# Kernel tuning notes

Hardware: AMD Instinct MI355X
Metric: run time of the kernel (lower is better)

## Reference

```python
import jax, jax.numpy as jnp
import numpy as np

PAD = -2.0
EPS = 1e-6

def _ln(x, g, b):
    m = jnp.mean(x, axis=-1, keepdims=True)
    v = jnp.var(x, axis=-1, keepdims=True)
    return (x - m) * jax.lax.rsqrt(v + EPS) * g + b

def setup_inputs() -> dict:
    key = jax.random.key(0)
    ks = jax.random.split(key, 8)
    B, N, D, H, E = 4, 2048, 256, 4, 256
    x = jax.random.normal(ks[0], (B, N, D), dtype=jnp.float32)
    mask = jnp.where(jax.random.uniform(ks[1], (B, N)) < 0.9, 1.0, PAD).astype(jnp.float32)
    Wq = jax.random.normal(ks[2], (H, D, E), dtype=jnp.float32) * 0.02
    Wk = jax.random.normal(ks[3], (H, D, E), dtype=jnp.float32) * 0.02
    Wv = jax.random.normal(ks[4], (H, D, E), dtype=jnp.float32) * 0.02
    Wg = jax.random.uniform(ks[5], (H, D, E), dtype=jnp.float32, minval=-0.05, maxval=0.05)
    out_w = jax.random.normal(ks[6], (E * H, E), dtype=jnp.float32) * 0.02
    out_b = jnp.zeros((E,), dtype=jnp.float32)
    ones = jnp.ones((E,), dtype=jnp.float32)
    zeros = jnp.zeros((E,), dtype=jnp.float32)
    return {"x": x, "mask": mask, "Wq": Wq, "Wk": Wk, "Wv": Wv, "Wg": Wg,
            "out_w": out_w, "out_b": out_b,
            "g_in": ones, "b_in": zeros, "g_res": ones, "b_res": zeros,
            "g_out": ones, "b_out": zeros}

def reference(x, mask, Wq, Wk, Wv, Wg, out_w, out_b, g_in, b_in, g_res, b_res, g_out, b_out):
    B, N, D = x.shape
    H, _, E = Wq.shape
    m = jnp.where(mask == PAD, 0.0, 1.0)            # [B,N]
    x_norm = _ln(x, g_in, b_in)                      # [B,N,D]
    q = jnp.einsum('bnd,hde->hbne', x_norm, Wq)
    k = jnp.einsum('bmd,hde->hbme', x_norm, Wk)
    v = jnp.einsum('bmd,hde->hbme', x_norm, Wv)
    scale = 1.0 / jnp.sqrt(jnp.float32(E))
    att = jnp.einsum('hbne,hbme->hbnm', q, k) * scale  # [H,B,N,N]
    amask = m[:, :, None] * m[:, None, :]              # outer-product mask [B,N,N]
    att = att + (1.0 - amask)[None] * -1e9
    att = jax.nn.softmax(att, axis=-1) * amask[None]   # post-softmax renorm by mask
    out = jnp.einsum('hbnm,hbme->hbne', att, v)        # [H,B,N,E]
    gate = jax.nn.sigmoid(jnp.einsum('bnd,hde->hbne', x_norm, Wg))
    out = out * gate
    out = _ln(out + x[None], g_res, b_res)             # residual + LN per head
    out = jnp.transpose(out, (1, 2, 3, 0)).reshape(B, N, E * H)  # [B,N,E*H], e fastest then h
    out = out @ out_w + out_b + x
    out = _ln(out, g_out, b_out)
    out = out * m[:, :, None]
    return out
```

## Files before the change

### kernel.cpp

```cpp
#include <hip/hip_runtime.h>
#include <math.h>

#define B_SZ 4
#define N_SEQ 2048
#define D_DIM 256
#define H_HEADS 4
#define E_DIM 256
#define ROWS (B_SZ*N_SEQ)
#define PAD_TOK -2.0f
#define LN_EPS 1e-6f

typedef __attribute__((ext_vector_type(8))) short short8;
typedef __attribute__((ext_vector_type(4))) float f32x4;

static __device__ __forceinline__ unsigned short f2bf(float f){
  union { float f; unsigned u; } v; v.f = f;
  unsigned r = v.u + 0x7fffu + ((v.u >> 16) & 1u);
  return (unsigned short)(r >> 16);
}
static __device__ __forceinline__ float bf2f(unsigned short s){
  union { unsigned u; float f; } v; v.u = ((unsigned)s) << 16; return v.f;
}
static __device__ __forceinline__ f32x4 mfma16(short8 a, short8 b, f32x4 c){
  return __builtin_amdgcn_mfma_f32_16x16x32_bf16(a, b, c, 0, 0, 0);
}

#define GLOAD_LDS16(gsrc, ldst) \
  __builtin_amdgcn_global_load_lds((const __attribute__((address_space(1))) void*)(gsrc), \
                                   (__attribute__((address_space(3))) void*)(ldst), 16, 0, 0)

__global__ __launch_bounds__(256) void k_ln_in(
    const float* __restrict__ x, const float* __restrict__ mask,
    const float* __restrict__ g, const float* __restrict__ bta,
    unsigned short* __restrict__ xn, float* __restrict__ mval){
  int row = blockIdx.x * 4 + (threadIdx.x >> 6);
  int lane = threadIdx.x & 63;
  const float* xr = x + (size_t)row * D_DIM + lane * 4;
  f32x4 v = *reinterpret_cast<const f32x4*>(xr);
  float s = v[0]+v[1]+v[2]+v[3];
  float q = v[0]*v[0]+v[1]*v[1]+v[2]*v[2]+v[3]*v[3];
  #pragma unroll
  for (int m=1;m<64;m<<=1){ s += __shfl_xor(s,m,64); q += __shfl_xor(q,m,64); }
  float mean = s * (1.0f/D_DIM);
  float var  = q * (1.0f/D_DIM) - mean*mean;
  float rs = rsqrtf(var + LN_EPS);
  int c = lane*4;
  ushort4 o;
  o.x = f2bf((v[0]-mean)*rs*g[c+0] + bta[c+0]);
  o.y = f2bf((v[1]-mean)*rs*g[c+1] + bta[c+1]);
  o.z = f2bf((v[2]-mean)*rs*g[c+2] + bta[c+2]);
  o.w = f2bf((v[3]-mean)*rs*g[c+3] + bta[c+3]);
  *reinterpret_cast<ushort4*>(xn + (size_t)row*D_DIM + c) = o;
  if (lane == 0) mval[row] = (mask[row] == PAD_TOK) ? 0.0f : 1.0f;
}

__global__ __launch_bounds__(256) void k_prep_w(
    const float* __restrict__ Wq, const float* __restrict__ Wk,
    const float* __restrict__ Wv, const float* __restrict__ Wg,
    unsigned short* __restrict__ wt){
  int mat = blockIdx.z; int proj = mat >> 2, h = mat & 3;
  const float* W = (proj==0 ? Wq : (proj==1 ? Wk : (proj==2 ? Wv : Wg))) + (size_t)h * D_DIM * E_DIM;
  __shared__ float tile[64][65];
  int e0 = blockIdx.x*64, d0 = blockIdx.y*64;
  #pragma unroll
  for (int i=0;i<16;i++){
    int idx = threadIdx.x + i*256;
    int dl = idx >> 6, el = idx & 63;
    tile[dl][el] = W[(size_t)(d0+dl)*E_DIM + e0 + el];
  }
  __syncthreads();
  #pragma unroll
  for (int i=0;i<16;i++){
    int idx = threadIdx.x + i*256;
    int el = idx >> 6, dl = idx & 63;
    wt[((size_t)mat*E_DIM + e0+el)*D_DIM + d0+dl] = f2bf(tile[dl][el]);
  }
}

__global__ __launch_bounds__(256) void k_prep_ow(
    const float* __restrict__ out_w, unsigned short* __restrict__ owt){
  int c0 = blockIdx.x*64;
  int col0 = blockIdx.y*64;
  int hh = c0 >> 8; int e0 = c0 & 255;
  __shared__ float tile[64][65];
  #pragma unroll
  for (int i=0;i<16;i++){
    int idx = threadIdx.x + i*256;
    int el = idx>>6, cl = idx&63;
    tile[el][cl] = out_w[(size_t)((e0+el)*H_HEADS + hh)*E_DIM + col0+cl];
  }
  __syncthreads();
  #pragma unroll
  for (int i=0;i<16;i++){
    int idx = threadIdx.x + i*256;
    int cl = idx>>6, el = idx&63;
    owt[(size_t)(col0+cl)*1024 + c0 + el] = f2bf(tile[el][cl]);
  }
}

__global__ __launch_bounds__(256,2) void k_proj(
    const unsigned short* __restrict__ xn, const unsigned short* __restrict__ wt,
    unsigned short* __restrict__ qb, unsigned short* __restrict__ kb,
    unsigned short* __restrict__ vtb, unsigned short* __restrict__ gpb){
  int mat = blockIdx.y; int proj = mat >> 2, h = mat & 3;
  int wv = threadIdx.x >> 6, lane = threadIdx.x & 63;
  int lr = lane & 15, lg = lane >> 4;
  int r0 = blockIdx.x * 128 + wv * 32;
  const unsigned short* wm = wt + (size_t)mat * D_DIM * E_DIM;
  short8 a[2][8];
  #pragma unroll
  for (int qr=0;qr<2;qr++){
    const unsigned short* arow = xn + (size_t)(r0 + qr*16 + lr) * D_DIM + lg*8;
    #pragma unroll
    for (int kk=0;kk<8;kk++) a[qr][kk] = *reinterpret_cast<const short8*>(arow + kk*32);
  }
  unsigned short* outp = (proj==0 ? qb : (proj==1 ? kb : gpb)) + (size_t)h * ROWS * E_DIM;
  #pragma unroll 2
  for (int nt=0; nt<16; nt++){
    f32x4 acc0 = f32x4{0.f,0.f,0.f,0.f};
    f32x4 acc1 = f32x4{0.f,0.f,0.f,0.f};
    const unsigned short* brow = wm + (size_t)(nt*16 + lr) * D_DIM + lg*8;
    #pragma unroll
    for (int kk=0;kk<8;kk++){
      short8 bfrag = *reinterpret_cast<const short8*>(brow + kk*32);
      acc0 = mfma16(a[0][kk], bfrag, acc0);
      acc1 = mfma16(a[1][kk], bfrag, acc1);
    }
    int col = nt*16 + lr;
    if (proj == 2){
      #pragma unroll
      for (int r=0;r<4;r++){
        int row0 = r0 + lg*4 + r;
        int row1 = row0 + 16;
        vtb[(((size_t)(h*B_SZ + (row0>>11))*E_DIM + col) << 11) + (row0 & 2047)] = f2bf(acc0[r]);
        vtb[(((size_t)(h*B_SZ + (row1>>11))*E_DIM + col) << 11) + (row1 & 2047)] = f2bf(acc1[r]);
      }
    } else {
      #pragma unroll
      for (int r=0;r<4;r++){
        int row0 = r0 + lg*4 + r;
        outp[(size_t)row0*E_DIM + col] = f2bf(acc0[r]);
        outp[(size_t)(row0+16)*E_DIM + col] = f2bf(acc1[r]);
      }
    }
  }
}

__global__ __launch_bounds__(256,2) void k_attn(
    const unsigned short* __restrict__ qb, const unsigned short* __restrict__ kb,
    const unsigned short* __restrict__ vt, const unsigned short* __restrict__ gp,
    const float* __restrict__ mval, const float* __restrict__ x,
    const float* __restrict__ g_res, const float* __restrict__ b_res,
    unsigned short* __restrict__ attout){
  int hb = blockIdx.y; int h = hb >> 2, bb = hb & 3;
  int tid = threadIdx.x;
  int wv = tid >> 6, lane = tid & 63;
  int lr = lane & 15, lg = lane >> 4;
  int n0 = blockIdx.x * 64 + wv * 16;
  const unsigned short* qm = qb + ((size_t)h * ROWS + (size_t)bb * N_SEQ) * E_DIM;
  const unsigned short* km = kb + ((size_t)h * ROWS + (size_t)bb * N_SEQ) * E_DIM;
  const unsigned short* vm = vt + ((size_t)(h * B_SZ + bb)) * E_DIM * N_SEQ;
  const unsigned short* gpm = gp + ((size_t)h * ROWS + (size_t)bb * N_SEQ) * E_DIM;
  const float* mrow = mval + bb * N_SEQ;

  __shared__ alignas(16) unsigned short Klds[2][32*256];
  __shared__ alignas(16) unsigned short Vlds[2][256][36];
  __shared__ alignas(16) unsigned short Plds[4][16][40];

  short8 qf[8];
  {
    const unsigned short* qrow = qm + (size_t)(n0 + lr) * E_DIM + lg * 8;
    #pragma unroll
    for (int kk=0;kk<8;kk++) qf[kk] = *reinterpret_cast<const short8*>(qrow + kk*32);
  }
  f32x4 o[16];
  #pragma unroll
  for (int i=0;i<16;i++) o[i] = f32x4{0.f,0.f,0.f,0.f};
  float mrun[4], lrun[4];
  #pragma unroll
  for (int r=0;r<4;r++){ mrun[r] = -1.0e30f; lrun[r] = 0.f; }

  {
    const char* kg = (const char*)km;
    #pragma unroll
    for (int i=0;i<4;i++){
      int c = tid + i*256; int krow = c >> 5;
      unsigned off = ((unsigned)(c*16)) ^ ((unsigned)((krow&7)<<4));
      GLOAD_LDS16(kg + off, (char*)(&Klds[0][0]) + c*16);
    }
    const unsigned short* vr = vm + (size_t)tid * N_SEQ;
    short8 v0[4];
    #pragma unroll
    for (int i=0;i<4;i++) v0[i] = *reinterpret_cast<const short8*>(vr + i*8);
    #pragma unroll
    for (int i=0;i<4;i++) *reinterpret_cast<short8*>(&Vlds[0][tid][i*8]) = v0[i];
  }
  __syncthreads();

  int cur = 0;
  for (int kt=0; kt<N_SEQ/32; kt++){
    int nxt = cur ^ 1;
    short8 vreg[4];
    if (kt < N_SEQ/32 - 1){
      const char* kg = (const char*)(km + (size_t)(kt+1)*32*E_DIM);
      #pragma unroll
      for (int i=0;i<4;i++){
        int c = tid + i*256; int krow = c >> 5;
        unsigned off = ((unsigned)(c*16)) ^ ((unsigned)((krow&7)<<4));
        GLOAD_LDS16(kg + off, (char*)(&Klds[nxt][0]) + c*16);
      }
      const unsigned short* vr = vm + (size_t)tid * N_SEQ + (kt+1)*32;
      #pragma unroll
      for (int i=0;i<4;i++) vreg[i] = *reinterpret_cast<const short8*>(vr + i*8);
    }
    const char* kbase = (const char*)(&Klds[cur][0]);
    f32x4 s0 = f32x4{0.f,0.f,0.f,0.f}, s1v = f32x4{0.f,0.f,0.f,0.f};
    unsigned swz = (unsigned)((lr&7)<<4);
    #pragma unroll
    for (int kk=0;kk<8;kk++){
      short8 b0 = *reinterpret_cast<const short8*>(kbase + ((unsigned)(lr*512 + kk*64 + lg*16) ^ swz));
      short8 b1 = *reinterpret_cast<const short8*>(kbase + ((unsigned)((16+lr)*512 + kk*64 + lg*16) ^ swz));
      s0  = mfma16(qf[kk], b0, s0);
      s1v = mfma16(qf[kk], b1, s1v);
    }
    float mk0 = (mrow[kt*32 + lr] - 1.0f) * 1e9f;
    float mk1 = (mrow[kt*32 + 16 + lr] - 1.0f) * 1e9f;
    float p0[4], p1[4], tmax[4];
    #pragma unroll
    for (int r=0;r<4;r++){
      p0[r] = s0[r]*0.0625f + mk0;
      p1[r] = s1v[r]*0.0625f + mk1;
      tmax[r] = fmaxf(p0[r], p1[r]);
    }
    #pragma unroll
    for (int m=1;m<16;m<<=1){
      #pragma unroll
      for (int r=0;r<4;r++) tmax[r] = fmaxf(tmax[r], __shfl_xor(tmax[r], m, 16));
    }
    bool need = false;
    #pragma unroll
    for (int r=0;r<4;r++) need = need || (tmax[r] > mrun[r] + 8.0f);
    if (__any((int)need)){
      #pragma unroll
      for (int r=0;r<4;r++){
        float mnew = fmaxf(mrun[r], tmax[r]);
        float alpha = __expf(mrun[r] - mnew);
        mrun[r] = mnew;
        lrun[r] *= alpha;
        #pragma unroll
        for (int i=0;i<16;i++) o[i][r] *= alpha;
      }
    }
    float rsum[4];
    #pragma unroll
    for (int r=0;r<4;r++){
      p0[r] = __expf(p0[r] - mrun[r]);
      p1[r] = __expf(p1[r] - mrun[r]);
      rsum[r] = p0[r] + p1[r];
    }
    #pragma unroll
    for (int m=1;m<16;m<<=1){
      #pragma unroll
      for (int r=0;r<4;r++) rsum[r] += __shfl_xor(rsum[r], m, 16);
    }
    #pragma unroll
    for (int r=0;r<4;r++) lrun[r] += rsum[r];
    #pragma unroll
    for (int r=0;r<4;r++){
      Plds[wv][lg*4+r][lr]      = f2bf(p0[r]);
      Plds[wv][lg*4+r][16+lr]   = f2bf(p1[r]);
    }
    short8 pa = *reinterpret_cast<const short8*>(&Plds[wv][lr][lg*8]);
    #pragma unroll
    for (int et=0;et<16;et++){
      short8 bv = *reinterpret_cast<const short8*>(&Vlds[cur][et*16 + lr][lg*8]);
      o[et] = mfma16(pa, bv, o[et]);
    }
    if (kt < N_SEQ/32 - 1){
      #pragma unroll
      for (int i=0;i<4;i++) *reinterpret_cast<short8*>(&Vlds[nxt][tid][i*8]) = vreg[i];
    }
    __syncthreads();
    cur = nxt;
  }
  float inv[4], mm_[4], rs_[4];
  #pragma unroll
  for (int r=0;r<4;r++) inv[r] = (lrun[r] > 0.f) ? (1.0f / lrun[r]) : 0.f;
  float s1_[4] = {0,0,0,0}, s2_[4] = {0,0,0,0};
  #pragma unroll
  for (int et=0;et<16;et++){
    int col = et*16 + lr;
    #pragma unroll
    for (int r=0;r<4;r++){
      int n = n0 + lg*4 + r;
      float ov = o[et][r] * inv[r];
      float gpre = bf2f(gpm[(size_t)n*E_DIM + col]);
      float gate = 1.0f / (1.0f + __expf(-gpre));
      float val = ov * gate + x[((size_t)(bb*N_SEQ + n))*D_DIM + col];
      o[et][r] = val;
      s1_[r] += val; s2_[r] += val*val;
    }
  }
  #pragma unroll
  for (int m=1;m<16;m<<=1){
    #pragma unroll
    for (int r=0;r<4;r++){ s1_[r] += __shfl_xor(s1_[r], m, 16); s2_[r] += __shfl_xor(s2_[r], m, 16); }
  }
  #pragma unroll
  for (int r=0;r<4;r++){
    float mean = s1_[r] * (1.0f/E_DIM);
    float var  = s2_[r] * (1.0f/E_DIM) - mean*mean;
    mm_[r] = mean; rs_[r] = rsqrtf(var + LN_EPS);
  }
  #pragma unroll
  for (int et=0;et<16;et++){
    int col = et*16 + lr;
    float gr = g_res[col], br = b_res[col];
    #pragma unroll
    for (int r=0;r<4;r++){
      int n = n0 + lg*4 + r;
      float y = (o[et][r] - mm_[r]) * rs_[r] * gr + br;
      attout[((size_t)(bb*N_SEQ + n))*1024 + h*256 + col] = f2bf(y);
    }
  }
}

__global__ __launch_bounds__(128) void k_final(
    const unsigned short* __restrict__ attout, const unsigned short* __restrict__ owt,
    const float* __restrict__ out_b, const float* __restrict__ x,
    const float* __restrict__ g_out, const float* __restrict__ b_out,
    const float* __restrict__ mval, float* __restrict__ out){
  int wv = threadIdx.x >> 6, lane = threadIdx.x & 63;
  int lr = lane & 15, lg = lane >> 4;
  int r0 = blockIdx.x * 32 + wv*16;
  f32x4 acc[16];
  #pragma unroll
  for (int i=0;i<16;i++) acc[i] = f32x4{0.f,0.f,0.f,0.f};
  const unsigned short* arow = attout + (size_t)(r0 + lr)*1024 + lg*8;
  for (int kg=0; kg<4; kg++){
    short8 a[8];
    #pragma unroll
    for (int kk=0;kk<8;kk++) a[kk] = *reinterpret_cast<const short8*>(arow + kg*256 + kk*32);
    #pragma unroll
    for (int nt=0;nt<16;nt++){
      const unsigned short* brow = owt + (size_t)(nt*16 + lr)*1024 + kg*256 + lg*8;
      #pragma unroll
      for (int kk=0;kk<8;kk++){
        short8 bfrag = *reinterpret_cast<const short8*>(brow + kk*32);
        acc[nt] = mfma16(a[kk], bfrag, acc[nt]);
      }
    }
  }
  float s1_[4]={0,0,0,0}, s2_[4]={0,0,0,0};
  #pragma unroll
  for (int nt=0;nt<16;nt++){
    int col = nt*16 + lr;
    float ob = out_b[col];
    #pragma unroll
    for (int r=0;r<4;r++){
      int row = r0 + lg*4 + r;
      float val = acc[nt][r] + ob + x[(size_t)row*D_DIM + col];
      acc[nt][r] = val;
      s1_[r]+=val; s2_[r]+=val*val;
    }
  }
  #pragma unroll
  for (int m=1;m<16;m<<=1){
    #pragma unroll
    for (int r=0;r<4;r++){ s1_[r]+=__shfl_xor(s1_[r],m,16); s2_[r]+=__shfl_xor(s2_[r],m,16); }
  }
  float mm_[4], rs_[4];
  #pragma unroll
  for (int r=0;r<4;r++){
    float mean = s1_[r]*(1.0f/E_DIM);
    float var  = s2_[r]*(1.0f/E_DIM) - mean*mean;
    mm_[r]=mean; rs_[r]=rsqrtf(var + LN_EPS);
  }
  #pragma unroll
  for (int nt=0;nt<16;nt++){
    int col = nt*16 + lr;
    float gg = g_out[col], bb2 = b_out[col];
    #pragma unroll
    for (int r=0;r<4;r++){
      int row = r0 + lg*4 + r;
      float y = ((acc[nt][r]-mm_[r])*rs_[r]*gg + bb2) * mval[row];
      out[(size_t)row*E_DIM + col] = y;
    }
  }
}

extern "C" void kernel_launch(void* const* d_in, const int* in_sizes, int n_in,
                              void* d_out, int out_size, void* d_ws, size_t ws_size,
                              hipStream_t stream) {
  const float* x     = (const float*)d_in[0];
  const float* mask  = (const float*)d_in[1];
  const float* Wq    = (const float*)d_in[2];
  const float* Wk    = (const float*)d_in[3];
  const float* Wv    = (const float*)d_in[4];
  const float* Wg    = (const float*)d_in[5];
  const float* out_w = (const float*)d_in[6];
  const float* out_b = (const float*)d_in[7];
  const float* g_in  = (const float*)d_in[8];
  const float* b_in  = (const float*)d_in[9];
  const float* g_res = (const float*)d_in[10];
  const float* b_res = (const float*)d_in[11];
  const float* g_out = (const float*)d_in[12];
  const float* b_out = (const float*)d_in[13];

  char* ws = (char*)d_ws;
  size_t off = 0;
  unsigned short* xn   = (unsigned short*)(ws + off); off += (size_t)ROWS * D_DIM * 2;
  float*          mval = (float*)(ws + off);          off += (size_t)ROWS * 4;
  unsigned short* wt   = (unsigned short*)(ws + off); off += (size_t)16 * D_DIM * E_DIM * 2;
  unsigned short* owt  = (unsigned short*)(ws + off); off += (size_t)E_DIM * 1024 * 2;
  unsigned short* qb   = (unsigned short*)(ws + off); off += (size_t)H_HEADS * ROWS * E_DIM * 2;
  unsigned short* kb   = (unsigned short*)(ws + off); off += (size_t)H_HEADS * ROWS * E_DIM * 2;
  unsigned short* vtb  = (unsigned short*)(ws + off); off += (size_t)H_HEADS * ROWS * E_DIM * 2;
  unsigned short* gpb  = (unsigned short*)(ws + off); off += (size_t)H_HEADS * ROWS * E_DIM * 2;
  unsigned short* attout = (unsigned short*)(ws + off); off += (size_t)ROWS * 1024 * 2;

  k_ln_in<<<dim3(ROWS/4), dim3(256), 0, stream>>>(x, mask, g_in, b_in, xn, mval);
  k_prep_w<<<dim3(4,4,16), dim3(256), 0, stream>>>(Wq, Wk, Wv, Wg, wt);
  k_prep_ow<<<dim3(16,4), dim3(256), 0, stream>>>(out_w, owt);
  k_proj<<<dim3(ROWS/128, 16), dim3(256), 0, stream>>>(xn, wt, qb, kb, vtb, gpb);
  k_attn<<<dim3(N_SEQ/64, H_HEADS*B_SZ), dim3(256), 0, stream>>>(qb, kb, vtb, gpb, mval, x, g_res, b_res, attout);
  k_final<<<dim3(ROWS/32), dim3(128), 0, stream>>>(attout, owt, out_b, x, g_out, b_out, mval, (float*)d_out);
}
```

Measured before the change: 364.5 us.

## Process 32 query rows per wave in attention, load V via direct LDS DMA

Each wave now handles two 16-row query groups, so every K and V fragment read from LDS feeds two MFMAs. This halves K/V global and LDS traffic per query row, and the grid shrinks to 256 blocks. V tiles are now staged with swizzled global-to-LDS loads instead of register round-trips, and blocks are remapped so neighbouring block ids share the same head and batch for L2 reuse. In exchange, register pressure doubles (launch bounds drop to 1 block per CU), and 256 blocks on a large GPU may leave CUs underused.

New measurement: 401.3 us. +10.1%, slower.

```diff
diff --git a/kernel.cpp b/kernel.cpp
--- a/kernel.cpp
+++ b/kernel.cpp
@@ -146,183 +146,234 @@
   }
 }
 
-__global__ __launch_bounds__(256,2) void k_attn(
+__global__ __launch_bounds__(256,1) void k_attn(
     const unsigned short* __restrict__ qb, const unsigned short* __restrict__ kb,
     const unsigned short* __restrict__ vt, const unsigned short* __restrict__ gp,
     const float* __restrict__ mval, const float* __restrict__ x,
     const float* __restrict__ g_res, const float* __restrict__ b_res,
     unsigned short* __restrict__ attout){
-  int hb = blockIdx.y; int h = hb >> 2, bb = hb & 3;
+  int id = blockIdx.x;
+  int hb = (id & 7) + ((id >> 7) << 3);
+  int h = hb >> 2, bbx = hb & 3;
+  int nblk = (id >> 3) & 15;
   int tid = threadIdx.x;
   int wv = tid >> 6, lane = tid & 63;
   int lr = lane & 15, lg = lane >> 4;
-  int n0 = blockIdx.x * 64 + wv * 16;
-  const unsigned short* qm = qb + ((size_t)h * ROWS + (size_t)bb * N_SEQ) * E_DIM;
-  const unsigned short* km = kb + ((size_t)h * ROWS + (size_t)bb * N_SEQ) * E_DIM;
-  const unsigned short* vm = vt + ((size_t)(h * B_SZ + bb)) * E_DIM * N_SEQ;
-  const unsigned short* gpm = gp + ((size_t)h * ROWS + (size_t)bb * N_SEQ) * E_DIM;
-  const float* mrow = mval + bb * N_SEQ;
+  int n0 = nblk * 128 + wv * 32;
+  const unsigned short* qm = qb + ((size_t)h * ROWS + (size_t)bbx * N_SEQ) * E_DIM;
+  const unsigned short* km = kb + ((size_t)h * ROWS + (size_t)bbx * N_SEQ) * E_DIM;
+  const unsigned short* vm = vt + ((size_t)(h * B_SZ + bbx)) * E_DIM * N_SEQ;
+  const unsigned short* gpm = gp + ((size_t)h * ROWS + (size_t)bbx * N_SEQ) * E_DIM;
+  const float* mrow = mval + bbx * N_SEQ;
 
   __shared__ alignas(16) unsigned short Klds[2][32*256];
-  __shared__ alignas(16) unsigned short Vlds[2][256][36];
-  __shared__ alignas(16) unsigned short Plds[4][16][40];
-
-  short8 qf[8];
+  __shared__ alignas(16) unsigned short Vlds[2][256*32];
+  __shared__ alignas(16) unsigned short Plds[4][32][40];
+
+  short8 qf0[8], qf1[8];
   {
-    const unsigned short* qrow = qm + (size_t)(n0 + lr) * E_DIM + lg * 8;
-    #pragma unroll
-    for (int kk=0;kk<8;kk++) qf[kk] = *reinterpret_cast<const short8*>(qrow + kk*32);
-  }
-  f32x4 o[16];
-  #pragma unroll
-  for (int i=0;i<16;i++) o[i] = f32x4{0.f,0.f,0.f,0.f};
-  float mrun[4], lrun[4];
-  #pragma unroll
-  for (int r=0;r<4;r++){ mrun[r] = -1.0e30f; lrun[r] = 0.f; }
-
-  {
-    const char* kg = (const char*)km;
-    #pragma unroll
-    for (int i=0;i<4;i++){
-      int c = tid + i*256; int krow = c >> 5;
-      unsigned off = ((unsigned)(c*16)) ^ ((unsigned)((krow&7)<<4));
-      GLOAD_LDS16(kg + off, (char*)(&Klds[0][0]) + c*16);
-    }
-    const unsigned short* vr = vm + (size_t)tid * N_SEQ;
-    short8 v0[4];
-    #pragma unroll
-    for (int i=0;i<4;i++) v0[i] = *reinterpret_cast<const short8*>(vr + i*8);
-    #pragma unroll
-    for (int i=0;i<4;i++) *reinterpret_cast<short8*>(&Vlds[0][tid][i*8]) = v0[i];
-  }
+    const unsigned short* qr0 = qm + (size_t)(n0 + lr) * E_DIM + lg * 8;
+    const unsigned short* qr1 = qm + (size_t)(n0 + 16 + lr) * E_DIM + lg * 8;
+    #pragma unroll
+    for (int kk=0;kk<8;kk++){
+      qf0[kk] = *reinterpret_cast<const short8*>(qr0 + kk*32);
+      qf1[kk] = *reinterpret_cast<const short8*>(qr1 + kk*32);
+    }
+  }
+  f32x4 o0[16], o1[16];
+  #pragma unroll
+  for (int i=0;i<16;i++){ o0[i] = f32x4{0.f,0.f,0.f,0.f}; o1[i] = f32x4{0.f,0.f,0.f,0.f}; }
+  float mr0[4], lr0_[4], mr1[4], lr1_[4];
+  #pragma unroll
+  for (int r=0;r<4;r++){ mr0[r] = -1.0e30f; lr0_[r] = 0.f; mr1[r] = -1.0e30f; lr1_[r] = 0.f; }
+
+  #define STAGE_K(buf, kt_) { \
+    const char* kgb = (const char*)(km + (size_t)(kt_)*32*E_DIM); \
+    _Pragma("unroll") \
+    for (int i=0;i<4;i++){ \
+      int c = tid + i*256; int krow = c >> 5; \
+      unsigned off = ((unsigned)(c*16)) ^ ((unsigned)((krow&7)<<4)); \
+      GLOAD_LDS16(kgb + off, (char*)(&Klds[buf][0]) + c*16); \
+    } }
+  #define STAGE_V(buf, kt_) { \
+    const char* vgb = (const char*)vm; \
+    _Pragma("unroll") \
+    for (int i=0;i<4;i++){ \
+      int c = tid + i*256; int e = c >> 2; \
+      unsigned w = (unsigned)(((c&3)*16) ^ ((e&3)<<4)); \
+      GLOAD_LDS16(vgb + (size_t)e*(N_SEQ*2) + (size_t)(kt_)*64 + w, \
+                  (char*)(&Vlds[buf][0]) + c*16); \
+    } }
+
+  STAGE_K(0, 0)
+  STAGE_V(0, 0)
   __syncthreads();
 
   int cur = 0;
   for (int kt=0; kt<N_SEQ/32; kt++){
     int nxt = cur ^ 1;
-    short8 vreg[4];
     if (kt < N_SEQ/32 - 1){
-      const char* kg = (const char*)(km + (size_t)(kt+1)*32*E_DIM);
-      #pragma unroll
-      for (int i=0;i<4;i++){
-        int c = tid + i*256; int krow = c >> 5;
-        unsigned off = ((unsigned)(c*16)) ^ ((unsigned)((krow&7)<<4));
-        GLOAD_LDS16(kg + off, (char*)(&Klds[nxt][0]) + c*16);
-      }
-      const unsigned short* vr = vm + (size_t)tid * N_SEQ + (kt+1)*32;
-      #pragma unroll
-      for (int i=0;i<4;i++) vreg[i] = *reinterpret_cast<const short8*>(vr + i*8);
+      STAGE_K(nxt, kt+1)
+      STAGE_V(nxt, kt+1)
     }
     const char* kbase = (const char*)(&Klds[cur][0]);
-    f32x4 s0 = f32x4{0.f,0.f,0.f,0.f}, s1v = f32x4{0.f,0.f,0.f,0.f};
+    f32x4 s00 = f32x4{0.f,0.f,0.f,0.f}, s01 = f32x4{0.f,0.f,0.f,0.f};
+    f32x4 s10 = f32x4{0.f,0.f,0.f,0.f}, s11 = f32x4{0.f,0.f,0.f,0.f};
     unsigned swz = (unsigned)((lr&7)<<4);
     #pragma unroll
     for (int kk=0;kk<8;kk++){
       short8 b0 = *reinterpret_cast<const short8*>(kbase + ((unsigned)(lr*512 + kk*64 + lg*16) ^ swz));
       short8 b1 = *reinterpret_cast<const short8*>(kbase + ((unsigned)((16+lr)*512 + kk*64 + lg*16) ^ swz));
-      s0  = mfma16(qf[kk], b0, s0);
-      s1v = mfma16(qf[kk], b1, s1v);
+      s00 = mfma16(qf0[kk], b0, s00);
+      s01 = mfma16(qf0[kk], b1, s01);
+      s10 = mfma16(qf1[kk], b0, s10);
+      s11 = mfma16(qf1[kk], b1, s11);
     }
     float mk0 = (mrow[kt*32 + lr] - 1.0f) * 1e9f;
     float mk1 = (mrow[kt*32 + 16 + lr] - 1.0f) * 1e9f;
-    float p0[4], p1[4], tmax[4];
-    #pragma unroll
-    for (int r=0;r<4;r++){
-      p0[r] = s0[r]*0.0625f + mk0;
-      p1[r] = s1v[r]*0.0625f + mk1;
-      tmax[r] = fmaxf(p0[r], p1[r]);
+    float p00[4], p01[4], t0[4];
+    #pragma unroll
+    for (int r=0;r<4;r++){
+      p00[r] = s00[r]*0.0625f + mk0;
+      p01[r] = s01[r]*0.0625f + mk1;
+      t0[r] = fmaxf(p00[r], p01[r]);
     }
     #pragma unroll
     for (int m=1;m<16;m<<=1){
       #pragma unroll
-      for (int r=0;r<4;r++) tmax[r] = fmaxf(tmax[r], __shfl_xor(tmax[r], m, 16));
-    }
-    bool need = false;
-    #pragma unroll
-    for (int r=0;r<4;r++) need = need || (tmax[r] > mrun[r] + 8.0f);
-    if (__any((int)need)){
-      #pragma unroll
-      for (int r=0;r<4;r++){
-        float mnew = fmaxf(mrun[r], tmax[r]);
-        float alpha = __expf(mrun[r] - mnew);
-        mrun[r] = mnew;
-        lrun[r] *= alpha;
+      for (int r=0;r<4;r++) t0[r] = fmaxf(t0[r], __shfl_xor(t0[r], m, 16));
+    }
+    bool need0 = (t0[0] > mr0[0]+8.0f) || (t0[1] > mr0[1]+8.0f) || (t0[2] > mr0[2]+8.0f) || (t0[3] > mr0[3]+8.0f);
+    if (__any((int)need0)){
+      #pragma unroll
+      for (int r=0;r<4;r++){
+        float mnew = fmaxf(mr0[r], t0[r]);
+        float alpha = __expf(mr0[r] - mnew);
+        mr0[r] = mnew; lr0_[r] *= alpha;
         #pragma unroll
-        for (int i=0;i<16;i++) o[i][r] *= alpha;
-      }
-    }
-    float rsum[4];
-    #pragma unroll
-    for (int r=0;r<4;r++){
-      p0[r] = __expf(p0[r] - mrun[r]);
-      p1[r] = __expf(p1[r] - mrun[r]);
-      rsum[r] = p0[r] + p1[r];
+        for (int i=0;i<16;i++) o0[i][r] *= alpha;
+      }
+    }
+    float rs0[4];
+    #pragma unroll
+    for (int r=0;r<4;r++){
+      p00[r] = __expf(p00[r] - mr0[r]);
+      p01[r] = __expf(p01[r] - mr0[r]);
+      rs0[r] = p00[r] + p01[r];
     }
     #pragma unroll
     for (int m=1;m<16;m<<=1){
       #pragma unroll
-      for (int r=0;r<4;r++) rsum[r] += __shfl_xor(rsum[r], m, 16);
-    }
-    #pragma unroll
-    for (int r=0;r<4;r++) lrun[r] += rsum[r];
-    #pragma unroll
-    for (int r=0;r<4;r++){
-      Plds[wv][lg*4+r][lr]      = f2bf(p0[r]);
-      Plds[wv][lg*4+r][16+lr]   = f2bf(p1[r]);
-    }
-    short8 pa = *reinterpret_cast<const short8*>(&Plds[wv][lr][lg*8]);
+      for (int r=0;r<4;r++) rs0[r] += __shfl_xor(rs0[r], m, 16);
+    }
+    #pragma unroll
+    for (int r=0;r<4;r++) lr0_[r] += rs0[r];
+    float p10[4], p11[4], t1[4];
+    #pragma unroll
+    for (int r=0;r<4;r++){
+      p10[r] = s10[r]*0.0625f + mk0;
+      p11[r] = s11[r]*0.0625f + mk1;
+      t1[r] = fmaxf(p10[r], p11[r]);
+    }
+    #pragma unroll
+    for (int m=1;m<16;m<<=1){
+      #pragma unroll
+      for (int r=0;r<4;r++) t1[r] = fmaxf(t1[r], __shfl_xor(t1[r], m, 16));
+    }
+    bool need1 = (t1[0] > mr1[0]+8.0f) || (t1[1] > mr1[1]+8.0f) || (t1[2] > mr1[2]+8.0f) || (t1[3] > mr1[3]+8.0f);
+    if (__any((int)need1)){
+      #pragma unroll
+      for (int r=0;r<4;r++){
+        float mnew = fmaxf(mr1[r], t1[r]);
+        float alpha = __expf(mr1[r] - mnew);
+        mr1[r] = mnew; lr1_[r] *= alpha;
+        #pragma unroll
+        for (int i=0;i<16;i++) o1[i][r] *= alpha;
+      }
+    }
+    float rs1[4];
+    #pragma unroll
+    for (int r=0;r<4;r++){
+      p10[r] = __expf(p10[r] - mr1[r]);
+      p11[r] = __expf(p11[r] - mr1[r]);
+      rs1[r] = p10[r] + p11[r];
+    }
+    #pragma unroll
+    for (int m=1;m<16;m<<=1){
+      #pragma unroll
+      for (int r=0;r<4;r++) rs1[r] += __shfl_xor(rs1[r], m, 16);
+    }
+    #pragma unroll
+    for (int r=0;r<4;r++) lr1_[r] += rs1[r];
+    #pragma unroll
+    for (int r=0;r<4;r++){
+      Plds[wv][lg*4+r][lr]       = f2bf(p00[r]);
+      Plds[wv][lg*4+r][16+lr]    = f2bf(p01[r]);
+      Plds[wv][16+lg*4+r][lr]    = f2bf(p10[r]);
+      Plds[wv][16+lg*4+r][16+lr] = f2bf(p11[r]);
+    }
+    short8 pa0 = *reinterpret_cast<const short8*>(&Plds[wv][lr][lg*8]);
+    short8 pa1 = *reinterpret_cast<const short8*>(&Plds[wv][16+lr][lg*8]);
+    const char* vbase = (const char*)(&Vlds[cur][0]);
+    unsigned vswz = (unsigned)((lr&3)<<4);
     #pragma unroll
     for (int et=0;et<16;et++){
-      short8 bv = *reinterpret_cast<const short8*>(&Vlds[cur][et*16 + lr][lg*8]);
-      o[et] = mfma16(pa, bv, o[et]);
-    }
-    if (kt < N_SEQ/32 - 1){
-      #pragma unroll
-      for (int i=0;i<4;i++) *reinterpret_cast<short8*>(&Vlds[nxt][tid][i*8]) = vreg[i];
+      short8 bv = *reinterpret_cast<const short8*>(vbase + ((unsigned)((et*16+lr)*64 + lg*16) ^ vswz));
+      o0[et] = mfma16(pa0, bv, o0[et]);
+      o1[et] = mfma16(pa1, bv, o1[et]);
     }
     __syncthreads();
     cur = nxt;
   }
-  float inv[4], mm_[4], rs_[4];
-  #pragma unroll
-  for (int r=0;r<4;r++) inv[r] = (lrun[r] > 0.f) ? (1.0f / lrun[r]) : 0.f;
-  float s1_[4] = {0,0,0,0}, s2_[4] = {0,0,0,0};
-  #pragma unroll
-  for (int et=0;et<16;et++){
-    int col = et*16 + lr;
-    #pragma unroll
-    for (int r=0;r<4;r++){
-      int n = n0 + lg*4 + r;
-      float ov = o[et][r] * inv[r];
-      float gpre = bf2f(gpm[(size_t)n*E_DIM + col]);
-      float gate = 1.0f / (1.0f + __expf(-gpre));
-      float val = ov * gate + x[((size_t)(bb*N_SEQ + n))*D_DIM + col];
-      o[et][r] = val;
-      s1_[r] += val; s2_[r] += val*val;
-    }
-  }
-  #pragma unroll
-  for (int m=1;m<16;m<<=1){
-    #pragma unroll
-    for (int r=0;r<4;r++){ s1_[r] += __shfl_xor(s1_[r], m, 16); s2_[r] += __shfl_xor(s2_[r], m, 16); }
-  }
-  #pragma unroll
-  for (int r=0;r<4;r++){
-    float mean = s1_[r] * (1.0f/E_DIM);
-    float var  = s2_[r] * (1.0f/E_DIM) - mean*mean;
-    mm_[r] = mean; rs_[r] = rsqrtf(var + LN_EPS);
-  }
-  #pragma unroll
-  for (int et=0;et<16;et++){
-    int col = et*16 + lr;
-    float gr = g_res[col], br = b_res[col];
-    #pragma unroll
-    for (int r=0;r<4;r++){
-      int n = n0 + lg*4 + r;
-      float y = (o[et][r] - mm_[r]) * rs_[r] * gr + br;
-      attout[((size_t)(bb*N_SEQ + n))*1024 + h*256 + col] = f2bf(y);
-    }
-  }
+  #pragma unroll
+  for (int grp=0; grp<2; grp++){
+    f32x4* o = grp ? o1 : o0;
+    float* lrn = grp ? lr1_ : lr0_;
+    int nb = n0 + grp*16;
+    float inv[4];
+    #pragma unroll
+    for (int r=0;r<4;r++) inv[r] = (lrn[r] > 0.f) ? (1.0f / lrn[r]) : 0.f;
+    float s1_[4] = {0,0,0,0}, s2_[4] = {0,0,0,0};
+    #pragma unroll
+    for (int et=0;et<16;et++){
+      int col = et*16 + lr;
+      #pragma unroll
+      for (int r=0;r<4;r++){
+        int n = nb + lg*4 + r;
+        float ov = o[et][r] * inv[r];
+        float gpre = bf2f(gpm[(size_t)n*E_DIM + col]);
+        float gate = 1.0f / (1.0f + __expf(-gpre));
+        float val = ov * gate + x[((size_t)(bbx*N_SEQ + n))*D_DIM + col];
+        o[et][r] = val;
+        s1_[r] += val; s2_[r] += val*val;
+      }
+    }
+    #pragma unroll
+    for (int m=1;m<16;m<<=1){
+      #pragma unroll
+      for (int r=0;r<4;r++){ s1_[r] += __shfl_xor(s1_[r], m, 16); s2_[r] += __shfl_xor(s2_[r], m, 16); }
+    }
+    float mm_[4], rsv[4];
+    #pragma unroll
+    for (int r=0;r<4;r++){
+      float mean = s1_[r] * (1.0f/E_DIM);
+      float var  = s2_[r] * (1.0f/E_DIM) - mean*mean;
+      mm_[r] = mean; rsv[r] = rsqrtf(var + LN_EPS);
+    }
+    #pragma unroll
+    for (int et=0;et<16;et++){
+      int col = et*16 + lr;
+      float gr = g_res[col], br = b_res[col];
+      #pragma unroll
+      for (int r=0;r<4;r++){
+        int n = nb + lg*4 + r;
+        float y = (o[et][r] - mm_[r]) * rsv[r] * gr + br;
+        attout[((size_t)(bbx*N_SEQ + n))*1024 + h*256 + col] = f2bf(y);
+      }
+    }
+  }
+  #undef STAGE_K
+  #undef STAGE_V
 }
 
 __global__ __launch_bounds__(128) void k_final(
@@ -423,6 +474,6 @@
   k_prep_w<<<dim3(4,4,16), dim3(256), 0, stream>>>(Wq, Wk, Wv, Wg, wt);
   k_prep_ow<<<dim3(16,4), dim3(256), 0, stream>>>(out_w, owt);
   k_proj<<<dim3(ROWS/128, 16), dim3(256), 0, stream>>>(xn, wt, qb, kb, vtb, gpb);
-  k_attn<<<dim3(N_SEQ/64, H_HEADS*B_SZ), dim3(256), 0, stream>>>(qb, kb, vtb, gpb, mval, x, g_res, b_res, attout);
+  k_attn<<<dim3(256), dim3(256), 0, stream>>>(qb, kb, vtb, gpb, mval, x, g_res, b_res, attout);
   k_final<<<dim3(ROWS/32), dim3(128), 0, stream>>>(attout, owt, out_b, x, g_out, b_out, mval, (float*)d_out);
 }
```

## Split attention over key halves with larger query tiles and a separate combine kernel

Applied to the files above, without the earlier changes.

Each attention wave now handles 32 query rows instead of 16 and loads 64-key K/V tiles into LDS with direct global-to-LDS loads, doubling reuse of each loaded K/V tile. The key range is split into two halves processed by separate blocks; unnormalised partial outputs and row sums go to a workspace, and a new combine kernel applies normalisation, gating, residual and LayerNorm. The online max tracking is dropped: exponentials are taken without subtracting a running max, which removes the shuffle reductions but relies on scores staying small enough not to overflow. The V-transpose store in the projection kernel is also staged through shared memory so it is written coalesced. The cost is an extra kernel launch, extra workspace traffic and the loss of K/V double buffering.

Result: slower. 460.1 us (+26.2%).

```diff
diff --git a/kernel.cpp b/kernel.cpp
--- a/kernel.cpp
+++ b/kernel.cpp
@@ -7,6 +7,7 @@
 #define H_HEADS 4
 #define E_DIM 256
 #define ROWS (B_SZ*N_SEQ)
+#define TOT_Q (H_HEADS*ROWS)
 #define PAD_TOK -2.0f
 #define LN_EPS 1e-6f
 
@@ -107,6 +108,7 @@
   int lr = lane & 15, lg = lane >> 4;
   int r0 = blockIdx.x * 128 + wv * 32;
   const unsigned short* wm = wt + (size_t)mat * D_DIM * E_DIM;
+  __shared__ unsigned short vtile[16][136];
   short8 a[2][8];
   #pragma unroll
   for (int qr=0;qr<2;qr++){
@@ -115,7 +117,8 @@
     for (int kk=0;kk<8;kk++) a[qr][kk] = *reinterpret_cast<const short8*>(arow + kk*32);
   }
   unsigned short* outp = (proj==0 ? qb : (proj==1 ? kb : gpb)) + (size_t)h * ROWS * E_DIM;
-  #pragma unroll 2
+  int bb_ = (blockIdx.x*128) >> 11;
+  int nbase = (blockIdx.x*128) & 2047;
   for (int nt=0; nt<16; nt++){
     f32x4 acc0 = f32x4{0.f,0.f,0.f,0.f};
     f32x4 acc1 = f32x4{0.f,0.f,0.f,0.f};
@@ -128,13 +131,17 @@
     }
     int col = nt*16 + lr;
     if (proj == 2){
+      __syncthreads();
       #pragma unroll
       for (int r=0;r<4;r++){
-        int row0 = r0 + lg*4 + r;
-        int row1 = row0 + 16;
-        vtb[(((size_t)(h*B_SZ + (row0>>11))*E_DIM + col) << 11) + (row0 & 2047)] = f2bf(acc0[r]);
-        vtb[(((size_t)(h*B_SZ + (row1>>11))*E_DIM + col) << 11) + (row1 & 2047)] = f2bf(acc1[r]);
-      }
+        vtile[lr][wv*32 + lg*4 + r]      = f2bf(acc0[r]);
+        vtile[lr][wv*32 + 16 + lg*4 + r] = f2bf(acc1[r]);
+      }
+      __syncthreads();
+      int el = threadIdx.x >> 4, nl = (threadIdx.x & 15) * 8;
+      short8 vv = *reinterpret_cast<const short8*>(&vtile[el][nl]);
+      *reinterpret_cast<short8*>(
+        vtb + ((size_t)(h*B_SZ + bb_)*E_DIM + nt*16 + el)*N_SEQ + nbase + nl) = vv;
     } else {
       #pragma unroll
       for (int r=0;r<4;r++){
@@ -148,180 +155,173 @@
 
 __global__ __launch_bounds__(256,2) void k_attn(
     const unsigned short* __restrict__ qb, const unsigned short* __restrict__ kb,
-    const unsigned short* __restrict__ vt, const unsigned short* __restrict__ gp,
-    const float* __restrict__ mval, const float* __restrict__ x,
-    const float* __restrict__ g_res, const float* __restrict__ b_res,
-    unsigned short* __restrict__ attout){
-  int hb = blockIdx.y; int h = hb >> 2, bb = hb & 3;
+    const unsigned short* __restrict__ vt, const float* __restrict__ mval,
+    unsigned short* __restrict__ po, float* __restrict__ lbuf){
+  int id = blockIdx.x;
+  int kh = id & 1;
+  int hb = (id >> 1) & 15;
+  int nblk = id >> 5;
+  int h = hb >> 2, bbx = hb & 3;
   int tid = threadIdx.x;
   int wv = tid >> 6, lane = tid & 63;
   int lr = lane & 15, lg = lane >> 4;
-  int n0 = blockIdx.x * 64 + wv * 16;
-  const unsigned short* qm = qb + ((size_t)h * ROWS + (size_t)bb * N_SEQ) * E_DIM;
-  const unsigned short* km = kb + ((size_t)h * ROWS + (size_t)bb * N_SEQ) * E_DIM;
-  const unsigned short* vm = vt + ((size_t)(h * B_SZ + bb)) * E_DIM * N_SEQ;
-  const unsigned short* gpm = gp + ((size_t)h * ROWS + (size_t)bb * N_SEQ) * E_DIM;
-  const float* mrow = mval + bb * N_SEQ;
-
-  __shared__ alignas(16) unsigned short Klds[2][32*256];
-  __shared__ alignas(16) unsigned short Vlds[2][256][36];
-  __shared__ alignas(16) unsigned short Plds[4][16][40];
-
-  short8 qf[8];
+  int n0 = nblk * 128 + wv * 32;
+  const unsigned short* qm = qb + ((size_t)h * ROWS + (size_t)bbx * N_SEQ) * E_DIM;
+  const unsigned short* km = kb + ((size_t)h * ROWS + (size_t)bbx * N_SEQ) * E_DIM;
+  const char* vmb = (const char*)(vt + ((size_t)(h * B_SZ + bbx)) * E_DIM * N_SEQ);
+  const float* mrow = mval + bbx * N_SEQ + kh * (N_SEQ/2);
+
+  __shared__ alignas(16) unsigned short Klds[64*256];
+  __shared__ alignas(16) unsigned short Vlds[256*64];
+  __shared__ alignas(16) unsigned short Plds[4][32*64];
+
+  short8 qf0[8], qf1[8];
   {
-    const unsigned short* qrow = qm + (size_t)(n0 + lr) * E_DIM + lg * 8;
-    #pragma unroll
-    for (int kk=0;kk<8;kk++) qf[kk] = *reinterpret_cast<const short8*>(qrow + kk*32);
-  }
-  f32x4 o[16];
-  #pragma unroll
-  for (int i=0;i<16;i++) o[i] = f32x4{0.f,0.f,0.f,0.f};
-  float mrun[4], lrun[4];
-  #pragma unroll
-  for (int r=0;r<4;r++){ mrun[r] = -1.0e30f; lrun[r] = 0.f; }
-
-  {
-    const char* kg = (const char*)km;
-    #pragma unroll
-    for (int i=0;i<4;i++){
-      int c = tid + i*256; int krow = c >> 5;
-      unsigned off = ((unsigned)(c*16)) ^ ((unsigned)((krow&7)<<4));
-      GLOAD_LDS16(kg + off, (char*)(&Klds[0][0]) + c*16);
-    }
-    const unsigned short* vr = vm + (size_t)tid * N_SEQ;
-    short8 v0[4];
-    #pragma unroll
-    for (int i=0;i<4;i++) v0[i] = *reinterpret_cast<const short8*>(vr + i*8);
-    #pragma unroll
-    for (int i=0;i<4;i++) *reinterpret_cast<short8*>(&Vlds[0][tid][i*8]) = v0[i];
-  }
-  __syncthreads();
-
-  int cur = 0;
-  for (int kt=0; kt<N_SEQ/32; kt++){
-    int nxt = cur ^ 1;
-    short8 vreg[4];
-    if (kt < N_SEQ/32 - 1){
-      const char* kg = (const char*)(km + (size_t)(kt+1)*32*E_DIM);
-      #pragma unroll
-      for (int i=0;i<4;i++){
-        int c = tid + i*256; int krow = c >> 5;
+    const unsigned short* qr0 = qm + (size_t)(n0 + lr) * E_DIM + lg * 8;
+    const unsigned short* qr1 = qm + (size_t)(n0 + 16 + lr) * E_DIM + lg * 8;
+    #pragma unroll
+    for (int kk=0;kk<8;kk++){
+      qf0[kk] = *reinterpret_cast<const short8*>(qr0 + kk*32);
+      qf1[kk] = *reinterpret_cast<const short8*>(qr1 + kk*32);
+    }
+  }
+  f32x4 o0[16], o1[16];
+  #pragma unroll
+  for (int i=0;i<16;i++){ o0[i] = f32x4{0.f,0.f,0.f,0.f}; o1[i] = f32x4{0.f,0.f,0.f,0.f}; }
+  float lp0[4] = {0.f,0.f,0.f,0.f}, lp1[4] = {0.f,0.f,0.f,0.f};
+  char* pbase = (char*)(&Plds[wv][0]);
+  unsigned swz = (unsigned)((lr&7)<<4);
+
+  for (int it=0; it<16; it++){
+    if (it) __syncthreads();
+    {
+      const char* kgb = (const char*)(km + ((size_t)(kh*(N_SEQ/2) + it*64))*E_DIM);
+      #pragma unroll
+      for (int i=0;i<8;i++){
+        int c = tid + i*256;
+        int krow = c >> 5;
         unsigned off = ((unsigned)(c*16)) ^ ((unsigned)((krow&7)<<4));
-        GLOAD_LDS16(kg + off, (char*)(&Klds[nxt][0]) + c*16);
-      }
-      const unsigned short* vr = vm + (size_t)tid * N_SEQ + (kt+1)*32;
-      #pragma unroll
-      for (int i=0;i<4;i++) vreg[i] = *reinterpret_cast<const short8*>(vr + i*8);
-    }
-    const char* kbase = (const char*)(&Klds[cur][0]);
-    f32x4 s0 = f32x4{0.f,0.f,0.f,0.f}, s1v = f32x4{0.f,0.f,0.f,0.f};
-    unsigned swz = (unsigned)((lr&7)<<4);
-    #pragma unroll
-    for (int kk=0;kk<8;kk++){
-      short8 b0 = *reinterpret_cast<const short8*>(kbase + ((unsigned)(lr*512 + kk*64 + lg*16) ^ swz));
-      short8 b1 = *reinterpret_cast<const short8*>(kbase + ((unsigned)((16+lr)*512 + kk*64 + lg*16) ^ swz));
-      s0  = mfma16(qf[kk], b0, s0);
-      s1v = mfma16(qf[kk], b1, s1v);
-    }
-    float mk0 = (mrow[kt*32 + lr] - 1.0f) * 1e9f;
-    float mk1 = (mrow[kt*32 + 16 + lr] - 1.0f) * 1e9f;
-    float p0[4], p1[4], tmax[4];
+        GLOAD_LDS16(kgb + off, (char*)Klds + c*16);
+      }
+      #pragma unroll
+      for (int i=0;i<8;i++){
+        int c = tid + i*256;
+        int e = c >> 3;
+        unsigned off = ((unsigned)((c&7)*16)) ^ ((unsigned)((e&7)<<4));
+        GLOAD_LDS16(vmb + (size_t)e*(N_SEQ*2) + (size_t)(kh*16+it)*128 + off,
+                    (char*)Vlds + c*16);
+      }
+    }
+    __syncthreads();
+    #pragma unroll
+    for (int ct=0; ct<4; ct++){
+      f32x4 s0 = f32x4{0.f,0.f,0.f,0.f}, s1 = f32x4{0.f,0.f,0.f,0.f};
+      const char* krow0 = (const char*)Klds + (ct*16+lr)*512;
+      #pragma unroll
+      for (int kk=0;kk<8;kk++){
+        short8 b = *reinterpret_cast<const short8*>(krow0 + (((unsigned)(kk*64 + lg*16)) ^ swz));
+        s0 = mfma16(qf0[kk], b, s0);
+        s1 = mfma16(qf1[kk], b, s1);
+      }
+      float mk = (mrow[it*64 + ct*16 + lr] - 1.0f) * 1e9f;
+      #pragma unroll
+      for (int r=0;r<4;r++){
+        float e0 = __expf(s0[r]*0.0625f + mk);
+        float e1 = __expf(s1[r]*0.0625f + mk);
+        lp0[r] += e0; lp1[r] += e1;
+        int row0 = lg*4 + r, row1 = 16 + lg*4 + r;
+        *(unsigned short*)(pbase + row0*128 + (((unsigned)(ct*32 + lr*2)) ^ ((unsigned)((row0&7)<<4)))) = f2bf(e0);
+        *(unsigned short*)(pbase + row1*128 + (((unsigned)(ct*32 + lr*2)) ^ ((unsigned)((row1&7)<<4)))) = f2bf(e1);
+      }
+    }
+    short8 pa0a = *reinterpret_cast<const short8*>(pbase + lr*128      + (((unsigned)(lg*16)) ^ swz));
+    short8 pa0b = *reinterpret_cast<const short8*>(pbase + lr*128      + (((unsigned)(64 + lg*16)) ^ swz));
+    short8 pa1a = *reinterpret_cast<const short8*>(pbase + (16+lr)*128 + (((unsigned)(lg*16)) ^ swz));
+    short8 pa1b = *reinterpret_cast<const short8*>(pbase + (16+lr)*128 + (((unsigned)(64 + lg*16)) ^ swz));
+    #pragma unroll
+    for (int et=0;et<16;et++){
+      const char* vrow = (const char*)Vlds + (et*16+lr)*128;
+      short8 bva = *reinterpret_cast<const short8*>(vrow + (((unsigned)(lg*16)) ^ swz));
+      short8 bvb = *reinterpret_cast<const short8*>(vrow + (((unsigned)(64 + lg*16)) ^ swz));
+      o0[et] = mfma16(pa0a, bva, o0[et]);
+      o0[et] = mfma16(pa0b, bvb, o0[et]);
+      o1[et] = mfma16(pa1a, bva, o1[et]);
+      o1[et] = mfma16(pa1b, bvb, o1[et]);
+    }
+  }
+  #pragma unroll
+  for (int m=1;m<16;m<<=1){
+    #pragma unroll
+    for (int r=0;r<4;r++){ lp0[r] += __shfl_xor(lp0[r], m, 16); lp1[r] += __shfl_xor(lp1[r], m, 16); }
+  }
+  size_t rowbase = (size_t)kh*TOT_Q + (size_t)hb*N_SEQ + n0;
+  if (lr == 0){
     #pragma unroll
     for (int r=0;r<4;r++){
-      p0[r] = s0[r]*0.0625f + mk0;
-      p1[r] = s1v[r]*0.0625f + mk1;
-      tmax[r] = fmaxf(p0[r], p1[r]);
-    }
-    #pragma unroll
-    for (int m=1;m<16;m<<=1){
-      #pragma unroll
-      for (int r=0;r<4;r++) tmax[r] = fmaxf(tmax[r], __shfl_xor(tmax[r], m, 16));
-    }
-    bool need = false;
-    #pragma unroll
-    for (int r=0;r<4;r++) need = need || (tmax[r] > mrun[r] + 8.0f);
-    if (__any((int)need)){
-      #pragma unroll
-      for (int r=0;r<4;r++){
-        float mnew = fmaxf(mrun[r], tmax[r]);
-        float alpha = __expf(mrun[r] - mnew);
-        mrun[r] = mnew;
-        lrun[r] *= alpha;
-        #pragma unroll
-        for (int i=0;i<16;i++) o[i][r] *= alpha;
-      }
-    }
-    float rsum[4];
+      lbuf[rowbase + lg*4 + r]      = lp0[r];
+      lbuf[rowbase + 16 + lg*4 + r] = lp1[r];
+    }
+  }
+  #pragma unroll
+  for (int et=0;et<16;et++){
     #pragma unroll
     for (int r=0;r<4;r++){
-      p0[r] = __expf(p0[r] - mrun[r]);
-      p1[r] = __expf(p1[r] - mrun[r]);
-      rsum[r] = p0[r] + p1[r];
-    }
-    #pragma unroll
-    for (int m=1;m<16;m<<=1){
-      #pragma unroll
-      for (int r=0;r<4;r++) rsum[r] += __shfl_xor(rsum[r], m, 16);
-    }
-    #pragma unroll
-    for (int r=0;r<4;r++) lrun[r] += rsum[r];
-    #pragma unroll
-    for (int r=0;r<4;r++){
-      Plds[wv][lg*4+r][lr]      = f2bf(p0[r]);
-      Plds[wv][lg*4+r][16+lr]   = f2bf(p1[r]);
-    }
-    short8 pa = *reinterpret_cast<const short8*>(&Plds[wv][lr][lg*8]);
-    #pragma unroll
-    for (int et=0;et<16;et++){
-      short8 bv = *reinterpret_cast<const short8*>(&Vlds[cur][et*16 + lr][lg*8]);
-      o[et] = mfma16(pa, bv, o[et]);
-    }
-    if (kt < N_SEQ/32 - 1){
-      #pragma unroll
-      for (int i=0;i<4;i++) *reinterpret_cast<short8*>(&Vlds[nxt][tid][i*8]) = vreg[i];
-    }
-    __syncthreads();
-    cur = nxt;
-  }
-  float inv[4], mm_[4], rs_[4];
-  #pragma unroll
-  for (int r=0;r<4;r++) inv[r] = (lrun[r] > 0.f) ? (1.0f / lrun[r]) : 0.f;
-  float s1_[4] = {0,0,0,0}, s2_[4] = {0,0,0,0};
-  #pragma unroll
-  for (int et=0;et<16;et++){
-    int col = et*16 + lr;
-    #pragma unroll
-    for (int r=0;r<4;r++){
-      int n = n0 + lg*4 + r;
-      float ov = o[et][r] * inv[r];
-      float gpre = bf2f(gpm[(size_t)n*E_DIM + col]);
-      float gate = 1.0f / (1.0f + __expf(-gpre));
-      float val = ov * gate + x[((size_t)(bb*N_SEQ + n))*D_DIM + col];
-      o[et][r] = val;
-      s1_[r] += val; s2_[r] += val*val;
-    }
-  }
-  #pragma unroll
-  for (int m=1;m<16;m<<=1){
-    #pragma unroll
-    for (int r=0;r<4;r++){ s1_[r] += __shfl_xor(s1_[r], m, 16); s2_[r] += __shfl_xor(s2_[r], m, 16); }
-  }
-  #pragma unroll
-  for (int r=0;r<4;r++){
-    float mean = s1_[r] * (1.0f/E_DIM);
-    float var  = s2_[r] * (1.0f/E_DIM) - mean*mean;
-    mm_[r] = mean; rs_[r] = rsqrtf(var + LN_EPS);
-  }
-  #pragma unroll
-  for (int et=0;et<16;et++){
-    int col = et*16 + lr;
-    float gr = g_res[col], br = b_res[col];
-    #pragma unroll
-    for (int r=0;r<4;r++){
-      int n = n0 + lg*4 + r;
-      float y = (o[et][r] - mm_[r]) * rs_[r] * gr + br;
-      attout[((size_t)(bb*N_SEQ + n))*1024 + h*256 + col] = f2bf(y);
-    }
+      po[(rowbase + lg*4 + r)*256 + et*16 + lr]      = f2bf(o0[et][r]);
+      po[(rowbase + 16 + lg*4 + r)*256 + et*16 + lr] = f2bf(o1[et][r]);
+    }
+  }
+}
+
+__global__ __launch_bounds__(256,2) void k_comb(
+    const unsigned short* __restrict__ po, const float* __restrict__ lbuf,
+    const unsigned short* __restrict__ gp, const float* __restrict__ x,
+    const float* __restrict__ g_res, const float* __restrict__ b_res,
+    unsigned short* __restrict__ attout){
+  int bx = blockIdx.x;
+  int hb = bx >> 5, sub = bx & 31;
+  int h = hb >> 2, bbx = hb & 3;
+  int t = threadIdx.x;
+  int rl = t >> 2, qc = t & 3;
+  int n = sub*64 + rl;
+  size_t grow = (size_t)hb*N_SEQ + n;
+  float l = lbuf[grow] + lbuf[(size_t)TOT_Q + grow];
+  float inv = (l > 0.f) ? 1.0f/l : 0.f;
+  int c0 = qc*64;
+  const unsigned short* p0 = po + grow*256 + c0;
+  const unsigned short* p1 = po + ((size_t)TOT_Q)*256 + grow*256 + c0;
+  const unsigned short* gr = gp + ((size_t)h*ROWS + (size_t)bbx*N_SEQ + n)*E_DIM + c0;
+  const float* xr = x + ((size_t)(bbx*N_SEQ + n))*D_DIM + c0;
+  float vals[64];
+  float s1 = 0.f, s2 = 0.f;
+  #pragma unroll
+  for (int ch=0; ch<8; ch++){
+    short8 a0 = *reinterpret_cast<const short8*>(p0 + ch*8);
+    short8 a1 = *reinterpret_cast<const short8*>(p1 + ch*8);
+    short8 gg = *reinterpret_cast<const short8*>(gr + ch*8);
+    #pragma unroll
+    for (int j=0;j<8;j++){
+      float v = (bf2f((unsigned short)a0[j]) + bf2f((unsigned short)a1[j])) * inv;
+      float gate = 1.0f/(1.0f + __expf(-bf2f((unsigned short)gg[j])));
+      float val = v*gate + xr[ch*8+j];
+      vals[ch*8+j] = val;
+      s1 += val; s2 += val*val;
+    }
+  }
+  s1 += __shfl_xor(s1,1,64); s2 += __shfl_xor(s2,1,64);
+  s1 += __shfl_xor(s1,2,64); s2 += __shfl_xor(s2,2,64);
+  float mean = s1*(1.0f/E_DIM);
+  float var  = s2*(1.0f/E_DIM) - mean*mean;
+  float rs = rsqrtf(var + LN_EPS);
+  unsigned short* ob = attout + ((size_t)(bbx*N_SEQ + n))*1024 + h*256 + c0;
+  #pragma unroll
+  for (int ch=0; ch<8; ch++){
+    short8 w;
+    #pragma unroll
+    for (int j=0;j<8;j++){
+      int col = c0 + ch*8 + j;
+      w[j] = (short)f2bf((vals[ch*8+j]-mean)*rs*g_res[col] + b_res[col]);
+    }
+    *reinterpret_cast<short8*>(ob + ch*8) = w;
   }
 }
 
@@ -418,11 +418,14 @@
   unsigned short* vtb  = (unsigned short*)(ws + off); off += (size_t)H_HEADS * ROWS * E_DIM * 2;
   unsigned short* gpb  = (unsigned short*)(ws + off); off += (size_t)H_HEADS * ROWS * E_DIM * 2;
   unsigned short* attout = (unsigned short*)(ws + off); off += (size_t)ROWS * 1024 * 2;
+  unsigned short* po   = (unsigned short*)(ws + off); off += (size_t)2 * TOT_Q * E_DIM * 2;
+  float*          lbuf = (float*)(ws + off);          off += (size_t)2 * TOT_Q * 4;
 
   k_ln_in<<<dim3(ROWS/4), dim3(256), 0, stream>>>(x, mask, g_in, b_in, xn, mval);
   k_prep_w<<<dim3(4,4,16), dim3(256), 0, stream>>>(Wq, Wk, Wv, Wg, wt);
   k_prep_ow<<<dim3(16,4), dim3(256), 0, stream>>>(out_w, owt);
   k_proj<<<dim3(ROWS/128, 16), dim3(256), 0, stream>>>(xn, wt, qb, kb, vtb, gpb);
-  k_attn<<<dim3(N_SEQ/64, H_HEADS*B_SZ), dim3(256), 0, stream>>>(qb, kb, vtb, gpb, mval, x, g_res, b_res, attout);
+  k_attn<<<dim3(512), dim3(256), 0, stream>>>(qb, kb, vtb, mval, po, lbuf);
+  k_comb<<<dim3(512), dim3(256), 0, stream>>>(po, lbuf, gpb, x, g_res, b_res, attout);
   k_final<<<dim3(ROWS/32), dim3(128), 0, stream>>>(attout, owt, out_b, x, g_out, b_out, mval, (float*)d_out);
 }
```
